# Optimization experiments

Measured on AMD Instinct MI355X. Metric: run time of the kernel, lower is better.

Reference implementation:

```python
import jax, jax.numpy as jnp
import numpy as np

G1, G2, G3 = 4.0, 5.0, 10.0   # cfg.SMOOTH.GAMMA1/2/3 (DAMSM defaults)
T_MOCO = 0.05
EPS = 1e-8


def _ce(logits, labels):
    # mean cross-entropy, labels are int class indices
    lp = jax.nn.log_softmax(logits, axis=-1)
    return -jnp.mean(jnp.take_along_axis(lp, labels[:, None], axis=1)[:, 0])


def _norm(x):
    return jnp.sqrt(jnp.sum(x * x, axis=-1, keepdims=True))


def setup_inputs() -> dict:
    key = jax.random.key(0)
    ks = jax.random.split(key, 8)
    B, T, NEF, H, K = 64, 32, 256, 17, 16384
    return {
        "cnn_code": jax.random.normal(ks[0], (B, NEF), jnp.float32),
        "rnn_code": jax.random.normal(ks[1], (B, NEF), jnp.float32),
        "img_features": jax.random.normal(ks[2], (B, NEF, H, H), jnp.float32),
        "words_emb": jax.random.normal(ks[3], (B, T, NEF), jnp.float32),
        "cnn_code_aug": jax.random.normal(ks[4], (B, NEF), jnp.float32),
        "rnn_code_aug": jax.random.normal(ks[5], (B, NEF), jnp.float32),
        "queue": jax.random.normal(ks[6], (NEF, K), jnp.float32),
        "queue_im": jax.random.normal(ks[7], (NEF, K), jnp.float32),
        "sentence_mask": jnp.ones((B, T), jnp.int32),
        "labels": jnp.arange(B, dtype=jnp.int32),
    }


def reference(cnn_code, rnn_code, img_features, words_emb, cnn_code_aug,
              rnn_code_aug, queue, queue_im, sentence_mask, labels):
    B = words_emb.shape[0]
    # ---------- local word-region attention loss (vectorized over the
    # per-sample python loop; sentence_mask is all-ones -> full length) ----------
    q = jnp.transpose(words_emb, (0, 2, 1))                   # [B, nef, T]
    ctx = img_features.reshape(B, img_features.shape[1], -1)  # [B, nef, S]
    # func_attention: scores[i,j,s,t] between query sample i and image j
    scores = jnp.einsum('jcs,ict->ijst', ctx, q)
    attn = jax.nn.softmax(scores, axis=3)        # softmax over words (queryL)
    attn = jax.nn.softmax(G1 * attn, axis=2)     # softmax over regions (sourceL)
    wC = jnp.einsum('jcs,ijst->ijct', ctx, attn)  # weighted context [i,j,nef,T]
    num = jnp.einsum('ict,ijct->ijt', q, wC)
    qn = jnp.sqrt(jnp.sum(q * q, axis=1))[:, None, :]         # [B,1,T]
    wn = jnp.sqrt(jnp.sum(wC * wC, axis=2))                   # [B,B,T]
    cos = num / jnp.clip(qn * wn, EPS, None)                  # [i,j,T]
    sim = jax.nn.logsumexp(G2 * cos, axis=2)                  # log(sum exp(G2*cos))
    S = sim.T * G3                                            # [j, i] as in original cat(dim=1)
    w_loss0 = _ce(S, labels)
    w_loss1 = _ce(S.T, labels)
    # ---------- global contrastive loss ----------
    cn = cnn_code / jnp.clip(_norm(cnn_code), EPS, None)
    rn = rnn_code / jnp.clip(_norm(rnn_code), EPS, None)
    can = cnn_code_aug / jnp.clip(_norm(cnn_code_aug), EPS, None)
    ran = rnn_code_aug / jnp.clip(_norm(rnn_code_aug), EPS, None)
    qz = jax.lax.stop_gradient(queue)
    qzi = jax.lax.stop_gradient(queue_im)
    zeros = jnp.zeros((B,), dtype=labels.dtype)
    log_it = jnp.concatenate([jnp.sum(cn * ran, -1, keepdims=True), cn @ qz], -1) / T_MOCO
    log_ti = jnp.concatenate([jnp.sum(rn * can, -1, keepdims=True), rn @ qzi], -1) / T_MOCO
    m_loss = (_ce(log_it, zeros) + _ce(log_ti, zeros)) / 2.0
    s0 = G3 * (cn @ rn.T)    # cosine(cnn, rnn) * GAMMA3
    s2 = G3 * (rn @ ran.T)   # cosine(rnn, rnn_aug) * GAMMA3
    loss0 = _ce(s0, labels)
    loss1 = _ce(s0.T, labels)
    loss2 = _ce(s2, labels)
    loss3 = _ce(s2.T, labels)
    return jnp.stack([w_loss0, w_loss1, loss0, loss1, m_loss, loss2, loss3])
```

## Files before the change

kernel.cpp:

```cpp
#include <hip/hip_runtime.h>
#include <hip/hip_bf16.h>
#include <math.h>

#define BB   64
#define TT   32
#define CC   256
#define KK   16384
#define G1c  4.0f
#define G2c  5.0f
#define G3c  10.0f
#define INV_T 20.0f
#define EPSF 1e-8f

#define WS_SIM 0
#define WS_S0  4096
#define WS_S2  8192
#define WS_CN  12288
#define WS_RN  28672
#define WS_CAN 45056
#define WS_RAN 61440
#define WS_QN  77824
#define WS_PM  79872
#define WS_PS  (WS_PM + 16384)
#define WS_CNT  (WS_PS + 16384)
#define WS_RNT  (WS_CNT + 16384)
#define WS_CANT (WS_RNT + 16384)
#define WS_RANT (WS_CANT + 16384)
#define WS_F32_TOTAL (WS_RANT + 16384)

#define CTXT_ELEMS (64*320*256)
#define WQ_ELEMS   (64*32*256)
#define WQ_OFF     CTXT_ELEMS
#define CNRN_OFF   (CTXT_ELEMS + WQ_ELEMS)

typedef __attribute__((ext_vector_type(8))) short short8;
typedef __attribute__((ext_vector_type(4))) short short4v;
typedef __attribute__((ext_vector_type(4))) float float4v;

__device__ __forceinline__ float4v mfma_bf16(short8 a, short8 b, float4v c) {
    return __builtin_amdgcn_mfma_f32_16x16x32_bf16(a, b, c, 0, 0, 0);
}

__device__ __forceinline__ short f2bf(float f) {
    union { float f; unsigned u; } x; x.f = f;
    unsigned r = x.u + 0x7FFFu + ((x.u >> 16) & 1u);
    return (short)(r >> 16);
}

__device__ __forceinline__ int swz13(int L) {
    return L ^ (((L>>10)&3)<<4) ^ ((((L>>6)&1) ^ ((L>>10)&1))<<3);
}

__global__ __launch_bounds__(256) void prep_kernel(
    const float* __restrict__ cnn, const float* __restrict__ rnn,
    const float* __restrict__ img, const float* __restrict__ wemb,
    const float* __restrict__ cnnA, const float* __restrict__ rnnA,
    float* __restrict__ W)
{
    int bid = blockIdx.x, tid = threadIdx.x;
    short* B16 = (short*)(W + WS_F32_TOTAL);
    short* ctxT = B16;
    short* wq   = B16 + WQ_OFF;
    short* cnrn = B16 + CNRN_OFF;

    if (bid < 256) {
        int mat = bid >> 6, row = bid & 63;
        const float* src = (mat==0)? cnn : (mat==1)? rnn : (mat==2)? cnnA : rnnA;
        float* dst  = W + ((mat==0)? WS_CN  : (mat==1)? WS_RN  : (mat==2)? WS_CAN  : WS_RAN);
        float* dstT = W + ((mat==0)? WS_CNT : (mat==1)? WS_RNT : (mat==2)? WS_CANT : WS_RANT);
        float v = src[row*256 + tid];
        float ss = v*v;
        for (int o=1;o<64;o<<=1) ss += __shfl_xor(ss,o);
        __shared__ float sc[4];
        if ((tid&63)==0) sc[tid>>6] = ss;
        __syncthreads();
        float tot = sc[0]+sc[1]+sc[2]+sc[3];
        float inv = 1.0f / fmaxf(sqrtf(tot), EPSF);
        float nv = v*inv;
        dst[row*256+tid] = nv;
        dstT[tid*64+row] = nv;
        if (mat < 2) cnrn[(mat*64+row)*256 + tid] = f2bf(nv);
    } else if (bid < 320) {
        int i = bid - 256;
        int t = tid >> 3, k = tid & 7;
        const float* wp = wemb + (i*32 + t)*256 + k*32;
        float ss = 0.f;
        for (int c=0;c<32;c++){ float v = wp[c]; ss += v*v; }
        ss += __shfl_xor(ss,1); ss += __shfl_xor(ss,2); ss += __shfl_xor(ss,4);
        if (k==0) W[WS_QN + i*32 + t] = sqrtf(ss);
    } else if (bid < 1600) {
        int b3 = bid - 320; int j = b3 / 20, mt20 = b3 % 20;
        int half = mt20 & 1;
        int s0 = mt20 * 16;
        __shared__ float tbuf[16*257];
        for (int idx = tid; idx < 4096; idx += 256) {
            int c = idx >> 4, sl = idx & 15, s = s0 + sl;
            float v = (s < 289) ? img[((size_t)(j*256 + c))*289 + s] : 0.0f;
            tbuf[sl*257 + c] = v;
        }
        __syncthreads();
        short* dst = ctxT + (size_t)j*81920 + (size_t)mt20*4096;
        for (int idx = tid; idx < 4096; idx += 256) {
            int v = half*4096 + idx;
            int L = swz13(v);
            int sl = ((L>>10)&3)*4 + ((L>>4)&3);
            int c  = ((L>>6)&15)*16 + (L&15);
            dst[idx] = f2bf(tbuf[sl*257 + c]);
        }
    } else {
        for (int idx = (bid-1600)*256 + tid; idx < WQ_ELEMS; idx += 64*256) {
            wq[idx] = f2bf(wemb[idx]);
        }
    }
}

__global__ __launch_bounds__(256, 2) void attn_moco_kernel(
    const float* __restrict__ queue, const float* __restrict__ queueIm,
    float* __restrict__ W)
{
    __shared__ __align__(16) short ctx_sc[8192];
    __shared__ __align__(16) short eTile[2][2][32][40];
    __shared__ float Dp[4][32], Np[4][32];
    __shared__ float wn2P[4][2][2][16];
    __shared__ float redm[4][64], reds[4][64];
    __shared__ float sa0[256], sa1[256];
    __shared__ float part[2][64][4];

    int bid = blockIdx.x, tid = threadIdx.x;
    int lane = tid & 63, wave = tid >> 6;
    int lo16 = lane & 15, quad = lane >> 4;

    const short* B16 = (const short*)(W + WS_F32_TOTAL);

    if (bid >= 320) {
        const short* ctxT = B16;
        const short* wq   = B16 + WQ_OFF;

        int abid = bid - 320;
        int j = abid >> 5, ip = abid & 31;
        int i_l = wave >> 1, mt = wave & 1;
        int i_g = ip*2 + i_l;

        short8 bq[2][8];
        {
            const short* p = wq + i_g*8192;
            #pragma unroll
            for (int nt2=0;nt2<2;nt2++)
                #pragma unroll
                for (int kk=0;kk<8;kk++)
                    bq[nt2][kk] = *(const short8*)(p + (nt2*16+lo16)*256 + kk*32 + quad*8);
        }

        float4v wacc[4][4];
        #pragma unroll
        for (int cm=0;cm<4;cm++)
            #pragma unroll
            for (int cb=0;cb<4;cb++) wacc[cm][cb] = (float4v){0.f,0.f,0.f,0.f};
        float D8[8], N8[8];
        #pragma unroll
        for (int u=0;u<8;u++){ D8[u]=0.f; N8[u]=0.f; }

        const short* ctxTj = ctxT + (size_t)j * 81920;

        int s4p = lo16 >> 2;
        int qh = quad >> 1, ql = quad & 1;
        int Lb = (mt*4 + s4p)*1024 + qh*64
               + (((lo16&3) ^ s4p) << 4)
               + ((ql ^ qh ^ (s4p&1)) << 3);
        const short* score_base = ctx_sc + Lb;
        int pcol = mt*16 + (lo16 & 12) + ((lo16 & 3) ^ s4p);
        unsigned trA = (unsigned)(unsigned long long)(const void*)(&ctx_sc[0])
                     + (unsigned)(quad*4096 + wave*512 + lo16*2);
        unsigned trB = trA ^ 16u;

        short8 pf[4];
        #pragma unroll
        for (int m=0;m<4;m++) pf[m] = *(const short8*)(ctxTj + tid*32 + m*8);
        short8* buf8 = (short8*)ctx_sc;

        for (int tile = 0; tile < 10; tile++) {
            #pragma unroll
            for (int m=0;m<4;m++) buf8[tid*4+m] = pf[m];
            __syncthreads();
            if (tile < 9) {
                const short* g = ctxTj + (tile+1)*8192 + tid*32;
                #pragma unroll
                for (int m=0;m<4;m++) pf[m] = *(const short8*)(g + m*8);
            }

            float4v a0 = {0.f,0.f,0.f,0.f}, a1 = {0.f,0.f,0.f,0.f};
            #pragma unroll
            for (int kk=0;kk<8;kk++) {
                short8 cf = *(const short8*)(score_base + kk*128);
                a0 = mfma_bf16(bq[0][kk], cf, a0);
                a1 = mfma_bf16(bq[1][kk], cf, a1);
            }

            short4v w00,w01,w10,w11,w20,w21,w30,w31;
            asm volatile("ds_read_b64_tr_b16 %0, %1 offset:0"    : "=v"(w00) : "v"(trA));
            asm volatile("ds_read_b64_tr_b16 %0, %1 offset:2048" : "=v"(w01) : "v"(trB));
            asm volatile("ds_read_b64_tr_b16 %0, %1 offset:128"  : "=v"(w10) : "v"(trB));
            asm volatile("ds_read_b64_tr_b16 %0, %1 offset:2176" : "=v"(w11) : "v"(trA));
            asm volatile("ds_read_b64_tr_b16 %0, %1 offset:256"  : "=v"(w20) : "v"(trA));
            asm volatile("ds_read_b64_tr_b16 %0, %1 offset:2304" : "=v"(w21) : "v"(trB));
            asm volatile("ds_read_b64_tr_b16 %0, %1 offset:384"  : "=v"(w30) : "v"(trB));
            asm volatile("ds_read_b64_tr_b16 %0, %1 offset:2432" : "=v"(w31) : "v"(trA));

            float mx = fmaxf(fmaxf(fmaxf(a0[0],a0[1]), fmaxf(a0[2],a0[3])),
                             fmaxf(fmaxf(a1[0],a1[1]), fmaxf(a1[2],a1[3])));
            mx = fmaxf(mx, __shfl_xor(mx,16));
            mx = fmaxf(mx, __shfl_xor(mx,32));
            float e0[4], e1[4]; float z = 0.f;
            #pragma unroll
            for (int r=0;r<4;r++) {
                e0[r] = __expf(a0[r]-mx); e1[r] = __expf(a1[r]-mx);
                z += e0[r] + e1[r];
            }
            z += __shfl_xor(z,16); z += __shfl_xor(z,32);
            float grinv = G1c / z;
            int sg = tile*32 + mt*16 + lo16;
            int eb = tile & 1;
            short* et = &eTile[eb][i_l][0][0];
            #pragma unroll
            for (int r=0;r<4;r++) {
                float ev0 = __expf(e0[r]*grinv);
                float ev1 = __expf(e1[r]*grinv);
                if (sg < 289) {
                    D8[r]   += ev0; N8[r]   += ev0*a0[r];
                    D8[4+r] += ev1; N8[4+r] += ev1*a1[r];
                }
                et[(quad*4+r)*40 + pcol]    = f2bf(ev0);
                et[(16+quad*4+r)*40 + pcol] = f2bf(ev1);
            }
            __syncthreads();
            __builtin_amdgcn_sched_barrier(0);

            short8 wa_[4];
            wa_[0] = (short8){w00[0],w00[1],w00[2],w00[3], w01[0],w01[1],w01[2],w01[3]};
            wa_[1] = (short8){w10[0],w10[1],w10[2],w10[3], w11[0],w11[1],w11[2],w11[3]};
            wa_[2] = (short8){w20[0],w20[1],w20[2],w20[3], w21[0],w21[1],w21[2],w21[3]};
            wa_[3] = (short8){w30[0],w30[1],w30[2],w30[3], w31[0],w31[1],w31[2],w31[3]};
            {
                const short8 bf00 = *(const short8*)&eTile[eb][0][lo16][quad*8];
                const short8 bf01 = *(const short8*)&eTile[eb][0][16+lo16][quad*8];
                const short8 bf10 = *(const short8*)&eTile[eb][1][lo16][quad*8];
                const short8 bf11 = *(const short8*)&eTile[eb][1][16+lo16][quad*8];
                #pragma unroll
                for (int cm=0;cm<4;cm++) {
                    wacc[cm][0] = mfma_bf16(wa_[cm], bf00, wacc[cm][0]);
                    wacc[cm][1] = mfma_bf16(wa_[cm], bf01, wacc[cm][1]);
                    wacc[cm][2] = mfma_bf16(wa_[cm], bf10, wacc[cm][2]);
                    wacc[cm][3] = mfma_bf16(wa_[cm], bf11, wacc[cm][3]);
                }
            }
        }

        #pragma unroll
        for (int u=0;u<8;u++) {
            float d = D8[u], n = N8[u];
            d += __shfl_xor(d,1); d += __shfl_xor(d,2);
            d += __shfl_xor(d,4); d += __shfl_xor(d,8);
            n += __shfl_xor(n,1); n += __shfl_xor(n,2);
            n += __shfl_xor(n,4); n += __shfl_xor(n,8);
            if (lo16 == 0) {
                int t = (u>>2)*16 + quad*4 + (u&3);
                Dp[wave][t] = d; Np[wave][t] = n;
            }
        }
        #pragma unroll
        for (int cb=0;cb<4;cb++) {
            float ss = 0.f;
            #pragma unroll
            for (int cm=0;cm<4;cm++)
                #pragma unroll
                for (int r=0;r<4;r++){ float v = wacc[cm][cb][r]; ss += v*v; }
            ss += __shfl_xor(ss,16);
            ss += __shfl_xor(ss,32);
            if (quad==0) wn2P[wave][cb>>1][cb&1][lo16] = ss;
        }
        __syncthreads();

        if (tid < 64) {
            int i_f = tid >> 5, t = tid & 31;
            int nt2 = t >> 4, lo = t & 15;
            float w2 = wn2P[0][i_f][nt2][lo] + wn2P[1][i_f][nt2][lo]
                     + wn2P[2][i_f][nt2][lo] + wn2P[3][i_f][nt2][lo];
            float D = Dp[i_f*2][t] + Dp[i_f*2+1][t];
            float N = Np[i_f*2][t] + Np[i_f*2+1][t];
            int i_gf = ip*2 + i_f;
            float qv = W[WS_QN + i_gf*32 + t];
            float numS = N/D;
            float wnS = sqrtf(w2)/D;
            float v = G2c * (numS / fmaxf(qv*wnS, EPSF));
            float mx = v;
            for (int o=1;o<32;o<<=1) mx = fmaxf(mx, __shfl_xor(mx,o));
            float e = __expf(v-mx);
            for (int o=1;o<32;o<<=1) e += __shfl_xor(e,o);
            if (t==0) W[WS_SIM + i_gf*64 + j] = mx + __logf(e);
        }
    } else if (bid < 256) {
        int mu = bid >> 7, ch = bid & 127;
        const float* Q = mu ? queueIm : queue;
        const short* Abf = B16 + CNRN_OFF + mu*16384;

        short8 afr[4][8];
        #pragma unroll
        for (int mt=0;mt<4;mt++)
            #pragma unroll
            for (int kk=0;kk<8;kk++)
                afr[mt][kk] = *(const short8*)(Abf + (mt*16+lo16)*256 + kk*32 + quad*8);

        float m16[16], s16[16];
        #pragma unroll
        for (int u=0;u<16;u++){ m16[u] = -1e30f; s16[u] = 0.f; }

        for (int t4 = 0; t4 < 2; t4++) {
            int colb = ch*128 + (wave*2 + t4)*16;
            float4v acc[4];
            #pragma unroll
            for (int mt=0;mt<4;mt++) acc[mt] = (float4v){0.f,0.f,0.f,0.f};
            for (int ks = 0; ks < 8; ks++) {
                short8 bfr;
                #pragma unroll
                for (int jj=0;jj<8;jj++) {
                    float bv = Q[(size_t)(ks*32 + quad*8 + jj)*KK + colb + lo16];
                    bfr[jj] = f2bf(bv);
                }
                #pragma unroll
                for (int mt=0;mt<4;mt++) acc[mt] = mfma_bf16(afr[mt][ks], bfr, acc[mt]);
            }
            #pragma unroll
            for (int mt=0;mt<4;mt++)
                #pragma unroll
                for (int r=0;r<4;r++) {
                    float v = acc[mt][r]*INV_T;
                    int u = mt*4+r;
                    float nm = fmaxf(m16[u], v);
                    s16[u] = s16[u]*__expf(m16[u]-nm) + __expf(v-nm);
                    m16[u] = nm;
                }
        }
        #pragma unroll
        for (int u=0;u<16;u++) {
            #pragma unroll
            for (int o=1;o<16;o<<=1) {
                float om = __shfl_xor(m16[u],o), os = __shfl_xor(s16[u],o);
                float nm = fmaxf(m16[u],om);
                s16[u] = s16[u]*__expf(m16[u]-nm) + os*__expf(om-nm);
                m16[u] = nm;
            }
        }
        if (lo16 == 0) {
            #pragma unroll
            for (int u=0;u<16;u++) {
                int row = (u>>2)*16 + quad*4 + (u&3);
                redm[wave][row] = m16[u]; reds[wave][row] = s16[u];
            }
        }
        __syncthreads();
        if (tid < 64) {
            float m = redm[0][tid], s = reds[0][tid];
            for (int w=1;w<4;w++) {
                float om = redm[w][tid], os = reds[w][tid];
                float nm = fmaxf(m,om);
                s = s*__expf(m-nm) + os*__expf(om-nm);
                m = nm;
            }
            W[WS_PM + mu*8192 + ch*64 + tid] = m;
            W[WS_PS + mu*8192 + ch*64 + tid] = s;
        }
    } else {
        int i = bid - 256;
        sa0[tid] = W[WS_CN + i*256 + tid];
        sa1[tid] = W[WS_RN + i*256 + tid];
        __syncthreads();
        const float* B0 = W + WS_RN;
        const float* B1v = W + WS_RAN;
        float av0 = sa0[tid], av1 = sa1[tid];
        for (int jj = 0; jj < 64; jj++) {
            float v0 = av0 * B0[jj*256 + tid];
            float v1 = av1 * B1v[jj*256 + tid];
            for (int o=1;o<64;o<<=1){ v0 += __shfl_xor(v0,o); v1 += __shfl_xor(v1,o); }
            if (lane==0){ part[0][jj][wave]=v0; part[1][jj][wave]=v1; }
        }
        __syncthreads();
        if (tid < 128) {
            int mat = tid>>6, jj = tid&63;
            float s = part[mat][jj][0]+part[mat][jj][1]+part[mat][jj][2]+part[mat][jj][3];
            W[(mat? WS_S2 : WS_S0) + i*64 + jj] = G3c * s;
        }
    }
}

__global__ __launch_bounds__(256) void final_kernel(
    const int* __restrict__ labels, float* __restrict__ W, float* __restrict__ out)
{
    int tid = threadIdx.x;
    __shared__ float mats[3][64][65];
    __shared__ float mmL[2][4][64], ssL[2][4][64];
    __shared__ float cearr[6][64];
    __shared__ float cemoco[128];

    for (int idx = tid; idx < 3*4096; idx += 256) {
        int t = idx >> 12, rem = idx & 4095;
        const float* src = W + (t==0 ? WS_SIM : (t==1 ? WS_S0 : WS_S2));
        mats[t][rem>>6][rem&63] = src[rem];
    }

    {
        int g = tid >> 6, r = tid & 63;
        for (int mu=0; mu<2; mu++) {
            float m = -1e30f, s = 0.f;
            for (int k=0; k<32; k++) {
                int ch = g*32 + k;
                float om = W[WS_PM + mu*8192 + ch*64 + r];
                float os = W[WS_PS + mu*8192 + ch*64 + r];
                float nm = fmaxf(m, om);
                s = s*__expf(m-nm) + os*__expf(om-nm);
                m = nm;
            }
            mmL[mu][g][r] = m; ssL[mu][g][r] = s;
        }
    }
    __syncthreads();

    if (tid < 128) {
        int mu = tid>>6, r = tid&63;
        float m = mmL[mu][0][r], s = ssL[mu][0][r];
        for (int g=1; g<4; g++) {
            float om = mmL[mu][g][r], os = ssL[mu][g][r];
            float nm = fmaxf(m, om);
            s = s*__expf(m-nm) + os*__expf(om-nm);
            m = nm;
        }
        const float* AT = W + (mu ? WS_RNT : WS_CNT);
        const float* BT = W + (mu ? WS_CANT : WS_RANT);
        float dot = 0.f;
        for (int c=0; c<256; c++) dot += AT[c*64 + r]*BT[c*64 + r];
        float v0 = dot*INV_T;
        float nm = fmaxf(m, v0);
        float S = s*__expf(m-nm) + __expf(v0-nm);
        cemoco[tid] = nm + __logf(S) - v0;
    }

    for (int pass=0; pass<2; pass++) {
        int cfg = pass*4 + (tid>>6);
        int row = tid&63;
        if (cfg < 6) {
            int mi; float scale; int colMajor;
            if (cfg==0){ mi=0; scale=G3c; colMajor=1; }
            else if (cfg==1){ mi=0; scale=G3c; colMajor=0; }
            else if (cfg==2){ mi=1; scale=1.f; colMajor=0; }
            else if (cfg==3){ mi=1; scale=1.f; colMajor=1; }
            else if (cfg==4){ mi=2; scale=1.f; colMajor=0; }
            else            { mi=2; scale=1.f; colMajor=1; }
            float mx = -1e30f;
            for (int x=0;x<64;x++) {
                float v = (colMajor? mats[mi][x][row] : mats[mi][row][x])*scale;
                mx = fmaxf(mx, v);
            }
            float se = 0.f;
            for (int x=0;x<64;x++) {
                float v = (colMajor? mats[mi][x][row] : mats[mi][row][x])*scale;
                se += __expf(v-mx);
            }
            int lbl = labels[row];
            float diag = (colMajor? mats[mi][lbl][row] : mats[mi][row][lbl])*scale;
            cearr[cfg][row] = mx + __logf(se) - diag;
        }
    }
    __syncthreads();

    if (tid < 7) {
        float r;
        if (tid == 4) {
            float s0=0.f, s1=0.f;
            for (int k=0;k<64;k++){ s0 += cemoco[k]; s1 += cemoco[64+k]; }
            r = (s0/64.f + s1/64.f)*0.5f;
        } else {
            int cfg = (tid < 4) ? tid : tid - 1;
            float s = 0.f;
            for (int k=0;k<64;k++) s += cearr[cfg][k];
            r = s/64.f;
        }
        out[tid] = r;
    }
}

extern "C" void kernel_launch(void* const* d_in, const int* in_sizes, int n_in,
                              void* d_out, int out_size, void* d_ws, size_t ws_size,
                              hipStream_t stream)
{
    const float* cnn   = (const float*)d_in[0];
    const float* rnn   = (const float*)d_in[1];
    const float* img   = (const float*)d_in[2];
    const float* wemb  = (const float*)d_in[3];
    const float* cnnA  = (const float*)d_in[4];
    const float* rnnA  = (const float*)d_in[5];
    const float* queue   = (const float*)d_in[6];
    const float* queueIm = (const float*)d_in[7];
    const int*   labels  = (const int*)d_in[9];
    float* W   = (float*)d_ws;
    float* out = (float*)d_out;

    prep_kernel<<<1664, 256, 0, stream>>>(cnn, rnn, img, wemb, cnnA, rnnA, W);
    attn_moco_kernel<<<2368, 256, 0, stream>>>(queue, queueIm, W);
    final_kernel<<<1, 256, 0, stream>>>(labels, W, out);
}
```

Before: 233.1 us.

## Double-buffer context tiles via direct global-to-LDS loads and raise occupancy

```diff
diff --git a/kernel.cpp b/kernel.cpp
--- a/kernel.cpp
+++ b/kernel.cpp
@@ -49,6 +49,15 @@
 
 __device__ __forceinline__ int swz13(int L) {
     return L ^ (((L>>10)&3)<<4) ^ ((((L>>6)&1) ^ ((L>>10)&1))<<3);
+}
+
+__device__ __forceinline__ void stage_tile(const short* g, short* l) {
+    #pragma unroll
+    for (int m = 0; m < 4; m++)
+        __builtin_amdgcn_global_load_lds(
+            (const __attribute__((address_space(1))) unsigned int*)(g + m*512),
+            (__attribute__((address_space(3))) unsigned int*)(l + m*512),
+            16, 0, 0);
 }
 
 __global__ __launch_bounds__(256) void prep_kernel(
@@ -100,12 +109,14 @@
         }
         __syncthreads();
         short* dst = ctxT + (size_t)j*81920 + (size_t)mt20*4096;
-        for (int idx = tid; idx < 4096; idx += 256) {
-            int v = half*4096 + idx;
+        for (int idx4 = tid; idx4 < 1024; idx4 += 256) {
+            int v = half*4096 + idx4*4;
             int L = swz13(v);
             int sl = ((L>>10)&3)*4 + ((L>>4)&3);
             int c  = ((L>>6)&15)*16 + (L&15);
-            dst[idx] = f2bf(tbuf[sl*257 + c]);
+            const float* tb = &tbuf[sl*257 + c];
+            short4v o = { f2bf(tb[0]), f2bf(tb[1]), f2bf(tb[2]), f2bf(tb[3]) };
+            *(short4v*)(dst + idx4*4) = o;
         }
     } else {
         for (int idx = (bid-1600)*256 + tid; idx < WQ_ELEMS; idx += 64*256) {
@@ -114,11 +125,11 @@
     }
 }
 
-__global__ __launch_bounds__(256, 2) void attn_moco_kernel(
+__global__ __launch_bounds__(256, 3) void attn_moco_kernel(
     const float* __restrict__ queue, const float* __restrict__ queueIm,
     float* __restrict__ W)
 {
-    __shared__ __align__(16) short ctx_sc[8192];
+    __shared__ __align__(16) short ctx_sc[2][8192];
     __shared__ __align__(16) short eTile[2][2][32][40];
     __shared__ float Dp[4][32], Np[4][32];
     __shared__ float wn2P[4][2][2][16];
@@ -167,26 +178,17 @@
         int Lb = (mt*4 + s4p)*1024 + qh*64
                + (((lo16&3) ^ s4p) << 4)
                + ((ql ^ qh ^ (s4p&1)) << 3);
-        const short* score_base = ctx_sc + Lb;
         int pcol = mt*16 + (lo16 & 12) + ((lo16 & 3) ^ s4p);
-        unsigned trA = (unsigned)(unsigned long long)(const void*)(&ctx_sc[0])
-                     + (unsigned)(quad*4096 + wave*512 + lo16*2);
-        unsigned trB = trA ^ 16u;
-
-        short8 pf[4];
-        #pragma unroll
-        for (int m=0;m<4;m++) pf[m] = *(const short8*)(ctxTj + tid*32 + m*8);
-        short8* buf8 = (short8*)ctx_sc;
+        unsigned trbase = (unsigned)(unsigned long long)(const void*)(&ctx_sc[0][0])
+                        + (unsigned)(quad*4096 + wave*512 + lo16*2);
+
+        stage_tile(ctxTj + 0*8192 + wave*2048 + lane*8, &ctx_sc[0][wave*2048]);
+        stage_tile(ctxTj + 1*8192 + wave*2048 + lane*8, &ctx_sc[1][wave*2048]);
+        __syncthreads();
 
         for (int tile = 0; tile < 10; tile++) {
-            #pragma unroll
-            for (int m=0;m<4;m++) buf8[tid*4+m] = pf[m];
-            __syncthreads();
-            if (tile < 9) {
-                const short* g = ctxTj + (tile+1)*8192 + tid*32;
-                #pragma unroll
-                for (int m=0;m<4;m++) pf[m] = *(const short8*)(g + m*8);
-            }
+            int cur = tile & 1;
+            const short* score_base = &ctx_sc[cur][0] + Lb;
 
             float4v a0 = {0.f,0.f,0.f,0.f}, a1 = {0.f,0.f,0.f,0.f};
             #pragma unroll
@@ -196,6 +198,8 @@
                 a1 = mfma_bf16(bq[1][kk], cf, a1);
             }
 
+            unsigned trA = trbase + (unsigned)(cur*16384);
+            unsigned trB = trA ^ 16u;
             short4v w00,w01,w10,w11,w20,w21,w30,w31;
             asm volatile("ds_read_b64_tr_b16 %0, %1 offset:0"    : "=v"(w00) : "v"(trA));
             asm volatile("ds_read_b64_tr_b16 %0, %1 offset:2048" : "=v"(w01) : "v"(trB));
@@ -219,8 +223,7 @@
             z += __shfl_xor(z,16); z += __shfl_xor(z,32);
             float grinv = G1c / z;
             int sg = tile*32 + mt*16 + lo16;
-            int eb = tile & 1;
-            short* et = &eTile[eb][i_l][0][0];
+            short* et = &eTile[cur][i_l][0][0];
             #pragma unroll
             for (int r=0;r<4;r++) {
                 float ev0 = __expf(e0[r]*grinv);
@@ -234,6 +237,9 @@
             }
             __syncthreads();
             __builtin_amdgcn_sched_barrier(0);
+            if (tile < 8)
+                stage_tile(ctxTj + (tile+2)*8192 + wave*2048 + lane*8,
+                           &ctx_sc[cur][wave*2048]);
 
             short8 wa_[4];
             wa_[0] = (short8){w00[0],w00[1],w00[2],w00[3], w01[0],w01[1],w01[2],w01[3]};
@@ -241,10 +247,10 @@
             wa_[2] = (short8){w20[0],w20[1],w20[2],w20[3], w21[0],w21[1],w21[2],w21[3]};
             wa_[3] = (short8){w30[0],w30[1],w30[2],w30[3], w31[0],w31[1],w31[2],w31[3]};
             {
-                const short8 bf00 = *(const short8*)&eTile[eb][0][lo16][quad*8];
-                const short8 bf01 = *(const short8*)&eTile[eb][0][16+lo16][quad*8];
-                const short8 bf10 = *(const short8*)&eTile[eb][1][lo16][quad*8];
-                const short8 bf11 = *(const short8*)&eTile[eb][1][16+lo16][quad*8];
+                const short8 bf00 = *(const short8*)&eTile[cur][0][lo16][quad*8];
+                const short8 bf01 = *(const short8*)&eTile[cur][0][16+lo16][quad*8];
+                const short8 bf10 = *(const short8*)&eTile[cur][1][lo16][quad*8];
+                const short8 bf11 = *(const short8*)&eTile[cur][1][16+lo16][quad*8];
                 #pragma unroll
                 for (int cm=0;cm<4;cm++) {
                     wacc[cm][0] = mfma_bf16(wa_[cm], bf00, wacc[cm][0]);
@@ -303,23 +309,24 @@
         const float* Q = mu ? queueIm : queue;
         const short* Abf = B16 + CNRN_OFF + mu*16384;
 
-        short8 afr[4][8];
-        #pragma unroll
-        for (int mt=0;mt<4;mt++)
-            #pragma unroll
-            for (int kk=0;kk<8;kk++)
-                afr[mt][kk] = *(const short8*)(Abf + (mt*16+lo16)*256 + kk*32 + quad*8);
-
         float m16[16], s16[16];
         #pragma unroll
         for (int u=0;u<16;u++){ m16[u] = -1e30f; s16[u] = 0.f; }
 
-        for (int t4 = 0; t4 < 2; t4++) {
-            int colb = ch*128 + (wave*2 + t4)*16;
-            float4v acc[4];
-            #pragma unroll
-            for (int mt=0;mt<4;mt++) acc[mt] = (float4v){0.f,0.f,0.f,0.f};
-            for (int ks = 0; ks < 8; ks++) {
+        float4v acc[2][4];
+        #pragma unroll
+        for (int t4=0;t4<2;t4++)
+            #pragma unroll
+            for (int mt=0;mt<4;mt++) acc[t4][mt] = (float4v){0.f,0.f,0.f,0.f};
+
+        for (int ks = 0; ks < 8; ks++) {
+            short8 afr[4];
+            #pragma unroll
+            for (int mt=0;mt<4;mt++)
+                afr[mt] = *(const short8*)(Abf + (mt*16+lo16)*256 + ks*32 + quad*8);
+            #pragma unroll
+            for (int t4 = 0; t4 < 2; t4++) {
+                int colb = ch*128 + (wave*2 + t4)*16;
                 short8 bfr;
                 #pragma unroll
                 for (int jj=0;jj<8;jj++) {
@@ -327,19 +334,21 @@
                     bfr[jj] = f2bf(bv);
                 }
                 #pragma unroll
-                for (int mt=0;mt<4;mt++) acc[mt] = mfma_bf16(afr[mt][ks], bfr, acc[mt]);
-            }
+                for (int mt=0;mt<4;mt++) acc[t4][mt] = mfma_bf16(afr[mt], bfr, acc[t4][mt]);
+            }
+        }
+        #pragma unroll
+        for (int t4=0;t4<2;t4++)
             #pragma unroll
             for (int mt=0;mt<4;mt++)
                 #pragma unroll
                 for (int r=0;r<4;r++) {
-                    float v = acc[mt][r]*INV_T;
+                    float v = acc[t4][mt][r]*INV_T;
                     int u = mt*4+r;
                     float nm = fmaxf(m16[u], v);
                     s16[u] = s16[u]*__expf(m16[u]-nm) + __expf(v-nm);
                     m16[u] = nm;
                 }
-        }
         #pragma unroll
         for (int u=0;u<16;u++) {
             #pragma unroll
```

Result: slower. 302.9 us (+29.9%).
